# Kernel tuning notes

Measured on AMD Instinct MI355X. Metric: run time of the kernel, lower is better.

The kernel has to match this reference:

```python
import jax, jax.numpy as jnp
from jax import lax
import numpy as np
from jax.scipy.ndimage import map_coordinates

SIGMA = 1.0
RADIUS = 3          # from radius=(3,3); kernel size 7
TAU = (2.0, 2.0)
SCALE_FACTORS = (0.5, 1.0)
ITERATIONS = (2, 2)  # production uses (100,100); reduced for tractable reference
EPS = 1e-9
IN_EPS = 1e-5


def gaussian_kernel1d(sigma, radius):
    x = jnp.arange(-radius, radius + 1, dtype=jnp.float32)
    k = jnp.exp(-0.5 * (x / sigma) ** 2)
    return k / jnp.sum(k)


def smooth3d(vf, k):
    # separable depthwise Gaussian over the 3 spatial axes, SAME padding
    C = vf.shape[1]
    for ax in range(3):
        shp = [1, 1, 1]
        shp[ax] = k.shape[0]
        w = jnp.tile(k.reshape(1, 1, *shp), (C, 1, 1, 1, 1))
        vf = lax.conv_general_dilated(vf, w, (1, 1, 1), 'SAME',
                                      dimension_numbers=('NCDHW', 'OIDHW', 'NCDHW'),
                                      feature_group_count=C)
    return vf


def warp(img, vf):
    # img: [1,1,D,H,W], vf: [1,3,D,H,W] displacement in voxel units
    D, H, W = img.shape[2:]
    gz, gy, gx = jnp.meshgrid(jnp.arange(D, dtype=img.dtype),
                              jnp.arange(H, dtype=img.dtype),
                              jnp.arange(W, dtype=img.dtype), indexing='ij')
    coords = [gz + vf[0, 0], gy + vf[0, 1], gx + vf[0, 2]]
    out = map_coordinates(img[0, 0], coords, order=1, mode='nearest')
    return out[None, None]


def demon_forces(warped, fixed, spacing):
    # active demons: gradient of the (warped) moving image
    diff = warped - fixed  # [1,1,D,H,W]
    g = jnp.stack(jnp.gradient(warped[0, 0]), axis=0)[None]  # [1,3,D,H,W]
    g = g / spacing[None, :, None, None, None]
    denom = jnp.sum(g * g, axis=1, keepdims=True) + diff * diff
    return jnp.where(denom > EPS, diff * g / denom, 0.0)


def match_vf(vf, shape):
    # resize displacement field and rescale its magnitude per axis
    old = vf.shape[2:]
    if tuple(old) == tuple(shape):
        return vf
    scale = jnp.array([s1 / s2 for s1, s2 in zip(shape, old)], jnp.float32)
    vf = jax.image.resize(vf, vf.shape[:2] + tuple(shape), method='trilinear')
    return vf * scale[None, :, None, None, None]


def conv3d(x, w):
    return lax.conv_general_dilated(x, w, (1, 1, 1), 'SAME',
                                    dimension_numbers=('NCDHW', 'OIDHW', 'NCDHW'))


def instance_norm(x):
    m = jnp.mean(x, axis=(2, 3, 4), keepdims=True)
    v = jnp.var(x, axis=(2, 3, 4), keepdims=True)
    return (x - m) / jnp.sqrt(v + IN_EPS)


def mish(x):
    return x * jnp.tanh(jax.nn.softplus(x))


def setup_inputs() -> dict:
    key = jax.random.key(0)
    ks = jax.random.split(key, 8)
    D = 96
    image = jax.random.normal(ks[0], (1, 1, D, D, D), jnp.float32)
    moving = jax.random.normal(ks[1], (1, 1, D, D, D), jnp.float32)
    mask = jnp.ones((1, 1, D, D, D), jnp.float32)
    spacing = jnp.ones((3,), jnp.float32)
    w1 = jax.random.normal(ks[2], (32, 5, 3, 3, 3), jnp.float32) * 0.05
    w2 = jax.random.normal(ks[3], (64, 32, 3, 3, 3), jnp.float32) * 0.05
    w3 = jax.random.normal(ks[4], (32, 64, 3, 3, 3), jnp.float32) * 0.05
    w4 = jax.random.normal(ks[5], (3, 32, 3, 3, 3), jnp.float32) * 0.05
    b4 = jnp.zeros((3,), jnp.float32)
    return {'image': image, 'mask': mask, 'moving': moving, 'spacing': spacing,
            'w1': w1, 'w2': w2, 'w3': w3, 'w4': w4, 'b4': b4}


def reference(image, mask, moving, spacing, w1, w2, w3, w4, b4):
    kernel = gaussian_kernel1d(SIGMA, RADIUS)
    full_shape = image.shape[2:]
    vf = None
    for lvl, (sf, n_it) in enumerate(zip(SCALE_FACTORS, ITERATIONS)):
        shp = tuple(int(s * sf) for s in full_shape)
        f = jax.image.resize(image, image.shape[:2] + shp, method='trilinear')
        m = jax.image.resize(mask, mask.shape[:2] + shp, method='nearest')
        mv = jax.image.resize(moving, moving.shape[:2] + shp, method='trilinear')
        if vf is None:
            vf = jnp.zeros((image.shape[0], 3) + shp, jnp.float32)
        else:
            vf = match_vf(vf, shp)
        tau = TAU[lvl]

        def body(i, vf, mv=mv, f=f, m=m, tau=tau):
            warped = warp(mv, vf)
            vf = vf + tau * demon_forces(warped, f, spacing) * m
            return smooth3d(vf, kernel)

        vf = lax.fori_loop(0, n_it, body, vf)

    # the iterative registration runs under torch.no_grad()
    vf = lax.stop_gradient(vf)
    warped_moving = lax.stop_gradient(warp(moving, vf))  # last level is full scale

    # correction CNN: Conv3d/InstanceNorm3d/Mish stack on [vf, image*mask, warped_moving]
    x = jnp.concatenate([vf, image * mask, warped_moving], axis=1)  # [1,5,D,H,W]
    x = mish(instance_norm(conv3d(x, w1)))
    x = mish(instance_norm(conv3d(x, w2)))
    x = mish(instance_norm(conv3d(x, w3)))
    correction = conv3d(x, w4) + b4[None, :, None, None, None]
    corrected_vf = smooth3d(vf + correction, kernel)

    vf = match_vf(vf, full_shape)
    corrected_vf = match_vf(corrected_vf, full_shape)
    corrected_warped_moving = warp(moving, corrected_vf)
    return corrected_warped_moving, corrected_vf, vf
```

## Files before the change

### kernel.cpp

```cpp
#include <hip/hip_runtime.h>
#include <hip/hip_bf16.h>
#include <math.h>

#define DEV __device__ __forceinline__

constexpr int D96 = 96;
constexpr int N96 = D96 * D96 * D96;
constexpr int D48 = 48;
constexpr int N48 = D48 * D48 * D48;

#define GW0 0.3990502796524549f
#define GW1 0.2420362293761143f
#define GW2 0.05400558262251696f
#define GW3 0.004433048175243745f

typedef __attribute__((ext_vector_type(8))) short s16x8;
typedef __attribute__((ext_vector_type(4))) short s16x4;
typedef __attribute__((ext_vector_type(4))) float f32x4;
typedef __attribute__((ext_vector_type(16))) float f32x16;

DEV int clampi(int v, int lo, int hi) { return v < lo ? lo : (v > hi ? hi : v); }

DEV short f2bf(float f) { __hip_bfloat16 h = __float2bfloat16(f); short s; __builtin_memcpy(&s, &h, 2); return s; }
DEV float bf2f(short s) { __hip_bfloat16 h; __builtin_memcpy(&h, &s, 2); return __bfloat162float(h); }

__global__ void k_downsample2x(const float* __restrict__ src, float* __restrict__ dst)
{
    int idx = blockIdx.x * blockDim.x + threadIdx.x;
    if (idx >= N48) return;
    int x = idx % D48, y = (idx / D48) % D48, z = idx / (D48 * D48);

    float wz[4], wy[4], wx[4];
    int jz[4], jy[4], jx[4];
    auto mk = [](int i, float* w, int* j) {
        const float base[4] = {0.125f, 0.375f, 0.375f, 0.125f};
        float s = 0.f;
        #pragma unroll
        for (int t = 0; t < 4; ++t) {
            int jj = 2 * i - 1 + t;
            bool v = (jj >= 0) && (jj < D96);
            j[t] = v ? jj : 0;
            w[t] = v ? base[t] : 0.f;
            s += w[t];
        }
        float inv = 1.f / s;
        #pragma unroll
        for (int t = 0; t < 4; ++t) w[t] *= inv;
    };
    mk(z, wz, jz); mk(y, wy, jy); mk(x, wx, jx);

    float acc = 0.f;
    #pragma unroll
    for (int a = 0; a < 4; ++a) {
        #pragma unroll
        for (int b = 0; b < 4; ++b) {
            float wab = wz[a] * wy[b];
            int rowoff = (jz[a] * D96 + jy[b]) * D96;
            #pragma unroll
            for (int c = 0; c < 4; ++c)
                acc += wab * wx[c] * src[rowoff + jx[c]];
        }
    }
    dst[idx] = acc;
}

__global__ void k_upsample_vf(const float* __restrict__ src, float* __restrict__ dst)
{
    int idx = blockIdx.x * blockDim.x + threadIdx.x;
    if (idx >= 3 * N96) return;
    int c = idx / N96;
    int s = idx - c * N96;
    int x = s % D96, y = (s / D96) % D96, z = s / (D96 * D96);

    auto mk = [](int i, int* j, float* w) {
        int k = i >> 1;
        if ((i & 1) == 0) { j[0] = k - 1; w[0] = 0.25f; j[1] = k; w[1] = 0.75f; }
        else              { j[0] = k;     w[0] = 0.75f; j[1] = k + 1; w[1] = 0.25f; }
        float sum = 0.f;
        #pragma unroll
        for (int t = 0; t < 2; ++t) {
            bool v = (j[t] >= 0) && (j[t] < D48);
            if (!v) { w[t] = 0.f; j[t] = 0; }
            sum += w[t];
        }
        float inv = 1.f / sum;
        w[0] *= inv; w[1] *= inv;
    };
    int jz[2], jy[2], jx[2]; float wz[2], wy[2], wx[2];
    mk(z, jz, wz); mk(y, jy, wy); mk(x, jx, wx);

    const float* p = src + (size_t)c * N48;
    float acc = 0.f;
    #pragma unroll
    for (int a = 0; a < 2; ++a)
        #pragma unroll
        for (int b = 0; b < 2; ++b) {
            float wab = wz[a] * wy[b];
            int rowoff = (jz[a] * D48 + jy[b]) * D48;
            acc += wab * (wx[0] * p[rowoff + jx[0]] + wx[1] * p[rowoff + jx[1]]);
        }
    dst[idx] = 2.f * acc;
}

__global__ void k_warp(const float* __restrict__ img, const float* __restrict__ vf,
                       float* __restrict__ out, int D)
{
    int N = D * D * D;
    int idx = blockIdx.x * blockDim.x + threadIdx.x;
    if (idx >= N) return;
    int x = idx % D, y = (idx / D) % D, z = idx / (D * D);
    float cz = z + vf[idx], cy = y + vf[N + idx], cx = x + vf[2 * N + idx];
    float fz = floorf(cz), fy = floorf(cy), fx = floorf(cx);
    float wz = cz - fz, wy = cy - fy, wx = cx - fx;
    int z0 = clampi((int)fz, 0, D - 1), z1 = clampi((int)fz + 1, 0, D - 1);
    int y0 = clampi((int)fy, 0, D - 1), y1 = clampi((int)fy + 1, 0, D - 1);
    int x0 = clampi((int)fx, 0, D - 1), x1 = clampi((int)fx + 1, 0, D - 1);
    float v000 = img[(z0 * D + y0) * D + x0], v001 = img[(z0 * D + y0) * D + x1];
    float v010 = img[(z0 * D + y1) * D + x0], v011 = img[(z0 * D + y1) * D + x1];
    float v100 = img[(z1 * D + y0) * D + x0], v101 = img[(z1 * D + y0) * D + x1];
    float v110 = img[(z1 * D + y1) * D + x0], v111 = img[(z1 * D + y1) * D + x1];
    float c00 = v000 + wx * (v001 - v000);
    float c01 = v010 + wx * (v011 - v010);
    float c10 = v100 + wx * (v101 - v100);
    float c11 = v110 + wx * (v111 - v110);
    float c0 = c00 + wy * (c01 - c00);
    float c1 = c10 + wy * (c11 - c10);
    out[idx] = c0 + wz * (c1 - c0);
}

__global__ void k_forces(const float* __restrict__ warped, const float* __restrict__ fixed,
                         const float* __restrict__ mask, const float* __restrict__ spacing,
                         float* __restrict__ vf, int D, int maskD, float tau)
{
    int N = D * D * D;
    int idx = blockIdx.x * blockDim.x + threadIdx.x;
    if (idx >= N) return;
    int x = idx % D, y = (idx / D) % D, z = idx / (D * D);
    float w0 = warped[idx];
    float diff = w0 - fixed[idx];
    int sZ = D * D, sY = D;
    float gz = (z == 0) ? warped[idx + sZ] - w0 : (z == D - 1) ? w0 - warped[idx - sZ]
               : 0.5f * (warped[idx + sZ] - warped[idx - sZ]);
    float gy = (y == 0) ? warped[idx + sY] - w0 : (y == D - 1) ? w0 - warped[idx - sY]
               : 0.5f * (warped[idx + sY] - warped[idx - sY]);
    float gx = (x == 0) ? warped[idx + 1] - w0 : (x == D - 1) ? w0 - warped[idx - 1]
               : 0.5f * (warped[idx + 1] - warped[idx - 1]);
    gz /= spacing[0]; gy /= spacing[1]; gx /= spacing[2];
    float denom = gz * gz + gy * gy + gx * gx + diff * diff;
    float m;
    if (D == maskD) m = mask[idx];
    else {
        float r = (float)maskD / (float)D;
        int mz = clampi((int)((z + 0.5f) * r), 0, maskD - 1);
        int my = clampi((int)((y + 0.5f) * r), 0, maskD - 1);
        int mx = clampi((int)((x + 0.5f) * r), 0, maskD - 1);
        m = mask[(mz * maskD + my) * maskD + mx];
    }
    if (denom > 1e-9f) {
        float sc = tau * diff / denom * m;
        vf[idx]         += sc * gz;
        vf[N + idx]     += sc * gy;
        vf[2 * N + idx] += sc * gx;
    }
}

__global__ __launch_bounds__(256, 2)
void k_smooth3(const float* __restrict__ src, float* __restrict__ dst, int D)
{
    __shared__ float B1[10648];
    __shared__ float B2[7744];
    float* B3 = B1;
    int nt = D >> 4;
    int b = blockIdx.x;
    int tx = b % nt, ty = (b / nt) % nt, tz = b / (nt * nt);
    int c = blockIdx.y;
    int N = D * D * D;
    const float* s = src + (size_t)c * N;
    float* d = dst + (size_t)c * N;
    int x0 = tx * 16, y0 = ty * 16, z0 = tz * 16;
    int tid = threadIdx.x;

    for (int l = tid; l < 10648; l += 256) {
        int xx = l % 22, yy = (l / 22) % 22, zz = l / 484;
        int gz = z0 + zz - 3, gy = y0 + yy - 3, gx = x0 + xx - 3;
        float v = 0.f;
        if ((unsigned)gz < (unsigned)D && (unsigned)gy < (unsigned)D && (unsigned)gx < (unsigned)D)
            v = s[((size_t)gz * D + gy) * D + gx];
        B1[l] = v;
    }
    __syncthreads();
    for (int l = tid; l < 16 * 484; l += 256) {
        int xx = l % 22, yy = (l / 22) % 22, zo = l / 484;
        int base = (zo + 3) * 484 + yy * 22 + xx;
        B2[l] = GW0 * B1[base]
              + GW1 * (B1[base - 484] + B1[base + 484])
              + GW2 * (B1[base - 968] + B1[base + 968])
              + GW3 * (B1[base - 1452] + B1[base + 1452]);
    }
    __syncthreads();
    for (int l = tid; l < 16 * 16 * 22; l += 256) {
        int xx = l % 22, yo = (l / 22) % 16, zo = l / 352;
        int base = zo * 484 + (yo + 3) * 22 + xx;
        B3[l] = GW0 * B2[base]
              + GW1 * (B2[base - 22] + B2[base + 22])
              + GW2 * (B2[base - 44] + B2[base + 44])
              + GW3 * (B2[base - 66] + B2[base + 66]);
    }
    __syncthreads();
    for (int l = tid; l < 4096; l += 256) {
        int xo = l % 16, yo = (l / 16) % 16, zo = l / 256;
        int base = zo * 352 + yo * 22 + xo + 3;
        float a = GW0 * B3[base]
                + GW1 * (B3[base - 1] + B3[base + 1])
                + GW2 * (B3[base - 2] + B3[base + 2])
                + GW3 * (B3[base - 3] + B3[base + 3]);
        d[((size_t)(z0 + zo) * D + (y0 + yo)) * D + (x0 + xo)] = a;
    }
}

__global__ void k_pack_cl(const float* __restrict__ vf, const float* __restrict__ image,
                          const float* __restrict__ mask, const float* __restrict__ warped,
                          short* __restrict__ xin8)
{
    int i = blockIdx.x * blockDim.x + threadIdx.x;
    if (i >= N96) return;
    s16x8 v;
    v[0] = f2bf(vf[i]); v[1] = f2bf(vf[N96 + i]); v[2] = f2bf(vf[2 * N96 + i]);
    v[3] = f2bf(image[i] * mask[i]); v[4] = f2bf(warped[i]);
    v[5] = 0; v[6] = 0; v[7] = 0;
    *reinterpret_cast<s16x8*>(&xin8[(size_t)i * 8]) = v;
}

__global__ void k_wreorder_all(const float* __restrict__ w1, const float* __restrict__ w2,
                               const float* __restrict__ w3, const float* __restrict__ w4,
                               short* __restrict__ r1, short* __restrict__ r2,
                               short* __restrict__ r3, short* __restrict__ r4)
{
    int i = blockIdx.x * 256 + threadIdx.x;
    const int S1 = 7168, S2 = 55296, S3 = 55296, S4 = 13824;
    const float* w; short* r; int CIN, CINP, COUT, COUTP;
    int idx = i;
    if (idx < S1)              { w = w1; r = r1; CIN = 5;  CINP = 8;  COUT = 32; COUTP = 32; }
    else if ((idx -= S1) < S2) { w = w2; r = r2; CIN = 32; CINP = 32; COUT = 64; COUTP = 64; }
    else if ((idx -= S2) < S3) { w = w3; r = r3; CIN = 64; CINP = 64; COUT = 32; COUTP = 32; }
    else if ((idx -= S3) < S4) { w = w4; r = r4; CIN = 32; CINP = 32; COUT = 3;  COUTP = 16; }
    else return;
    int j = idx & 7;
    int co = (idx >> 3) % COUTP;
    int kg = idx / (8 * COUTP);
    int k = kg * 8 + j;
    int off = k / CINP, ci = k % CINP;
    float v = 0.f;
    if (co < COUT && off < 27 && ci < CIN)
        v = w[((size_t)co * CIN + ci) * 27 + off];
    r[idx] = f2bf(v);
}

DEV float mishf(float f)
{
    float e = __expf(f);
    float t = 1.f + e;
    float u = t * t + 1.f;
    return f - 2.f * f * __builtin_amdgcn_rcpf(u);
}

__global__ __launch_bounds__(256, 4)
void k_conv1(const short* __restrict__ act, const short* __restrict__ Wr,
             short* __restrict__ outcl, float* __restrict__ part)
{
    constexpr int YH = 6, TN = 3, KS = 14;
    constexpr int TILE_G = 3 * YH * 98;
    __shared__ __align__(16) short tile[TILE_G * 8];
    float* red = (float*)tile;

    int b = blockIdx.x;
    int xcd = b & 7, bidx = b >> 3;
    int zblk = xcd * 12 + bidx / 24;
    int y0 = (bidx % 24) * 4;

    int tid = threadIdx.x;
    int lane = tid & 63, wave = tid >> 6;
    int ln31 = lane & 31, hi = lane >> 5;

    for (int i = tid; i < TILE_G; i += 256) {
        int xi = i % 98, yi = (i / 98) % YH, zi = i / (98 * YH);
        int gz = zblk + zi - 1, gy = y0 + yi - 1, gx = xi - 1;
        s16x8 v = {0, 0, 0, 0, 0, 0, 0, 0};
        if ((unsigned)gz < 96u && (unsigned)gy < 96u && (unsigned)gx < 96u)
            v = *reinterpret_cast<const s16x8*>(&act[(size_t)((gz * 96 + gy) * 96 + gx) * 8]);
        *reinterpret_cast<s16x8*>(&tile[i * 8]) = v;
    }
    __syncthreads();

    f32x16 acc[TN];
    #pragma unroll
    for (int i = 0; i < TN; ++i)
        #pragma unroll
        for (int e = 0; e < 16; ++e) acc[i][e] = 0.f;

    int xb_[TN];
    #pragma unroll
    for (int i = 0; i < TN; ++i) xb_[i] = i * 32 + ln31;

    #pragma unroll
    for (int ks = 0; ks < KS; ++ks) {
        s16x8 a = *reinterpret_cast<const s16x8*>(&Wr[((size_t)(ks * 2 + hi) * 32 + ln31) * 8]);
        int off = ks * 2 + hi; if (off > 26) off = 26;
        int dz = off / 9, r9 = off - dz * 9, dy = r9 / 3, dx = r9 - dy * 3;
        #pragma unroll
        for (int i = 0; i < TN; ++i) {
            int gi = (dz * YH + wave + dy) * 98 + xb_[i] + dx;
            s16x8 bf = *reinterpret_cast<const s16x8*>(&tile[gi * 8]);
            acc[i] = __builtin_amdgcn_mfma_f32_32x32x16_bf16(a, bf, acc[i], 0, 0, 0);
        }
    }

    float st_s[16], st_q[16];
    #pragma unroll
    for (int j = 0; j < 16; ++j) { st_s[j] = 0.f; st_q[j] = 0.f; }
    #pragma unroll
    for (int i = 0; i < TN; ++i)
        #pragma unroll
        for (int e = 0; e < 16; ++e) {
            float v = acc[i][e];
            st_s[e] += v; st_q[e] += v * v;
        }
    #pragma unroll
    for (int j = 0; j < 16; ++j) {
        #pragma unroll
        for (int o = 1; o <= 16; o <<= 1) {
            st_s[j] += __shfl_xor(st_s[j], o);
            st_q[j] += __shfl_xor(st_q[j], o);
        }
    }

    __syncthreads();
    #pragma unroll
    for (int i = 0; i < TN; ++i) {
        int x = xb_[i];
        #pragma unroll
        for (int q = 0; q < 4; ++q) {
            s16x4 pk;
            #pragma unroll
            for (int r = 0; r < 4; ++r) pk[r] = f2bf(acc[i][q * 4 + r]);
            int bo = (((wave * 96 + x) * 32 + q * 8 + hi * 4) * 2) ^ ((x & 3) << 4);
            *reinterpret_cast<s16x4*>((char*)tile + bo) = pk;
        }
    }
    __syncthreads();
    for (int t = tid; t < 4 * 96 * 4; t += 256) {
        int gran = t & 3;
        int x = (t >> 2) % 96;
        int row = t / (4 * 96);
        int bo = (((row * 96 + x) * 32) * 2 + gran * 16) ^ ((x & 3) << 4);
        s16x8 v = *reinterpret_cast<const s16x8*>((char*)tile + bo);
        int vox = ((zblk * 96) + y0 + row) * 96 + x;
        *reinterpret_cast<s16x8*>(&outcl[(size_t)vox * 32 + gran * 8]) = v;
    }

    __syncthreads();
    if (ln31 == 0) {
        int base = (wave * 2 + hi) * 16;
        #pragma unroll
        for (int j = 0; j < 16; ++j) {
            red[(base + j) * 2]     = st_s[j];
            red[(base + j) * 2 + 1] = st_q[j];
        }
    }
    __syncthreads();
    if (tid < 64) {
        int c = tid >> 1, sel = tid & 1;
        int q = (c >> 3) & 3, hic = (c >> 2) & 1, r = c & 3;
        int j = q * 4 + r;
        float v = 0.f;
        #pragma unroll
        for (int w = 0; w < 4; ++w)
            v += red[((w * 2 + hic) * 16 + j) * 2 + sel];
        part[((size_t)c * gridDim.x + blockIdx.x) * 2 + sel] = v;
    }
}

template <int CINP, int COUTP, int MINW>
__global__ __launch_bounds__(256, MINW)
void k_conv_v3(const short* __restrict__ act, const short* __restrict__ Wr,
               short* __restrict__ outcl, float* __restrict__ part)
{
    constexpr int G = CINP / 8;
    constexpr int HALVES = CINP / 32;
    constexpr int TM = COUTP / 32;
    constexpr int TN = 3;
    constexpr int YH = 6;
    constexpr int TILE_SH = YH * 98 * 32;
    constexpr int TR_SH = 4 * 96 * COUTP;
    constexpr int SH_SIZE = TILE_SH > TR_SH ? TILE_SH : TR_SH;
    __shared__ __align__(16) short tile[SH_SIZE];
    float* red = (float*)tile;

    int b = blockIdx.x;
    int xcd = b & 7, bidx = b >> 3;
    int zblk = xcd * 12 + bidx / 24;
    int y0 = (bidx % 24) * 4;

    int tid = threadIdx.x;
    int lane = tid & 63, wave = tid >> 6;
    int ln31 = lane & 31, hi = lane >> 5;

    int xb_[TN];
    #pragma unroll
    for (int i = 0; i < TN; ++i) xb_[i] = i * 32 + ln31;

    f32x16 acc[TN][TM];
    #pragma unroll
    for (int i = 0; i < TN; ++i)
        #pragma unroll
        for (int m = 0; m < TM; ++m)
            #pragma unroll
            for (int e = 0; e < 16; ++e) acc[i][m][e] = 0.f;

    for (int p = 0; p < 3; ++p) {
        int gz = zblk + p - 1;
        for (int h = 0; h < HALVES; ++h) {
            __syncthreads();
            for (int i = tid; i < YH * 98 * 4; i += 256) {
                int g = i & 3, xi = (i >> 2) % 98, yi = (i >> 2) / 98;
                int gy = y0 + yi - 1, gx = xi - 1;
                s16x8 v = {0, 0, 0, 0, 0, 0, 0, 0};
                if ((unsigned)gz < 96u && (unsigned)gy < 96u && (unsigned)gx < 96u)
                    v = *reinterpret_cast<const s16x8*>(
                        &act[(size_t)((gz * 96 + gy) * 96 + gx) * CINP + (h * 4 + g) * 8]);
                int slot = g ^ ((xi >> 1) & 3);
                *reinterpret_cast<s16x8*>(&tile[(((yi * 98 + xi) << 2) + slot) * 8]) = v;
            }
            __syncthreads();
            int kgbase = p * 9 * G + h * 4;
            #pragma unroll
            for (int ks = 0; ks < 18; ++ks) {
                int kg = kgbase + (ks >> 1) * G + (ks & 1) * 2 + hi;
                s16x8 A[TM];
                #pragma unroll
                for (int m = 0; m < TM; ++m)
                    A[m] = *reinterpret_cast<const s16x8*>(
                        &Wr[((size_t)kg * COUTP + m * 32 + ln31) * 8]);
                int dy = (ks >> 1) / 3, dx = (ks >> 1) % 3;
                int gl = (ks & 1) * 2 + hi;
                #pragma unroll
                for (int i = 0; i < TN; ++i) {
                    int xi = xb_[i] + dx;
                    int gi = (((wave + dy) * 98 + xi) << 2) + (gl ^ ((xi >> 1) & 3));
                    s16x8 bf = *reinterpret_cast<const s16x8*>(&tile[gi * 8]);
                    #pragma unroll
                    for (int m = 0; m < TM; ++m)
                        acc[i][m] = __builtin_amdgcn_mfma_f32_32x32x16_bf16(A[m], bf, acc[i][m], 0, 0, 0);
                }
            }
        }
    }

    float st_s[TM * 16], st_q[TM * 16];
    #pragma unroll
    for (int j = 0; j < TM * 16; ++j) { st_s[j] = 0.f; st_q[j] = 0.f; }
    #pragma unroll
    for (int i = 0; i < TN; ++i)
        #pragma unroll
        for (int m = 0; m < TM; ++m)
            #pragma unroll
            for (int e = 0; e < 16; ++e) {
                float v = acc[i][m][e];
                st_s[m * 16 + e] += v;
                st_q[m * 16 + e] += v * v;
            }
    #pragma unroll
    for (int j = 0; j < TM * 16; ++j) {
        #pragma unroll
        for (int o = 1; o <= 16; o <<= 1) {
            st_s[j] += __shfl_xor(st_s[j], o);
            st_q[j] += __shfl_xor(st_q[j], o);
        }
    }

    constexpr int XM = (COUTP == 64) ? 7 : 3;
    __syncthreads();
    #pragma unroll
    for (int i = 0; i < TN; ++i) {
        int x = xb_[i];
        #pragma unroll
        for (int m = 0; m < TM; ++m)
            #pragma unroll
            for (int q = 0; q < 4; ++q) {
                s16x4 pk;
                #pragma unroll
                for (int r = 0; r < 4; ++r) pk[r] = f2bf(acc[i][m][q * 4 + r]);
                int bo = (((wave * 96 + x) * COUTP + m * 32 + q * 8 + hi * 4) * 2) ^ ((x & XM) << 4);
                *reinterpret_cast<s16x4*>((char*)tile + bo) = pk;
            }
    }
    __syncthreads();
    constexpr int GR = COUTP / 8;
    for (int t = tid; t < 4 * 96 * GR; t += 256) {
        int gran = t % GR;
        int x = (t / GR) % 96;
        int row = t / (GR * 96);
        int bo = (((row * 96 + x) * COUTP) * 2 + gran * 16) ^ ((x & XM) << 4);
        s16x8 v = *reinterpret_cast<const s16x8*>((char*)tile + bo);
        int vox = ((zblk * 96) + y0 + row) * 96 + x;
        *reinterpret_cast<s16x8*>(&outcl[(size_t)vox * COUTP + gran * 8]) = v;
    }

    __syncthreads();
    if (ln31 == 0) {
        int base = (wave * 2 + hi) * (TM * 16);
        #pragma unroll
        for (int j = 0; j < TM * 16; ++j) {
            red[(base + j) * 2]     = st_s[j];
            red[(base + j) * 2 + 1] = st_q[j];
        }
    }
    __syncthreads();
    if (tid < COUTP * 2) {
        int c = tid >> 1, sel = tid & 1;
        int m = c >> 5, q = (c >> 3) & 3, hic = (c >> 2) & 1, r = c & 3;
        int j = m * 16 + q * 4 + r;
        float v = 0.f;
        #pragma unroll
        for (int w = 0; w < 4; ++w)
            v += red[((w * 2 + hic) * (TM * 16) + j) * 2 + sel];
        part[((size_t)c * gridDim.x + blockIdx.x) * 2 + sel] = v;
    }
}

__global__ __launch_bounds__(256, 4)
void k_conv4(const short* __restrict__ act, const short* __restrict__ Wr,
             const float* __restrict__ bias, const float* __restrict__ vf,
             float* __restrict__ corr, float* __restrict__ outvf)
{
    constexpr int YH = 6;
    __shared__ __align__(16) short tile[YH * 98 * 32];

    int b = blockIdx.x;
    int xcd = b & 7, bidx = b >> 3;
    int zblk = xcd * 12 + bidx / 24;
    int y0 = (bidx % 24) * 4;

    int tid = threadIdx.x;
    int lane = tid & 63, wave = tid >> 6;
    int ln15 = lane & 15, lg = lane >> 4;

    f32x4 acc[6];
    #pragma unroll
    for (int i = 0; i < 6; ++i) acc[i] = {0.f, 0.f, 0.f, 0.f};

    for (int p = 0; p < 3; ++p) {
        int gz = zblk + p - 1;
        __syncthreads();
        for (int i = tid; i < YH * 98 * 4; i += 256) {
            int g = i & 3, xi = (i >> 2) % 98, yi = (i >> 2) / 98;
            int gy = y0 + yi - 1, gx = xi - 1;
            s16x8 v = {0, 0, 0, 0, 0, 0, 0, 0};
            if ((unsigned)gz < 96u && (unsigned)gy < 96u && (unsigned)gx < 96u)
                v = *reinterpret_cast<const s16x8*>(
                    &act[(size_t)((gz * 96 + gy) * 96 + gx) * 32 + g * 8]);
            int slot = g ^ ((xi >> 1) & 3);
            *reinterpret_cast<s16x8*>(&tile[(((yi * 98 + xi) << 2) + slot) * 8]) = v;
        }
        __syncthreads();
        #pragma unroll
        for (int ks = 0; ks < 9; ++ks) {
            int kg = (p * 9 + ks) * 4 + lg;
            s16x8 a = *reinterpret_cast<const s16x8*>(&Wr[((size_t)kg * 16 + ln15) * 8]);
            int dy = ks / 3, dx = ks % 3;
            #pragma unroll
            for (int i = 0; i < 6; ++i) {
                int xi = i * 16 + ln15 + dx;
                int gi = (((wave + dy) * 98 + xi) << 2) + (lg ^ ((xi >> 1) & 3));
                s16x8 bf = *reinterpret_cast<const s16x8*>(&tile[gi * 8]);
                acc[i] = __builtin_amdgcn_mfma_f32_16x16x32_bf16(a, bf, acc[i], 0, 0, 0);
            }
        }
    }
    if (lg == 0) {
        #pragma unroll
        for (int i = 0; i < 6; ++i) {
            int vox = ((zblk * 96) + y0 + wave) * 96 + i * 16 + ln15;
            #pragma unroll
            for (int r = 0; r < 3; ++r) {
                float v = vf[(size_t)r * N96 + vox];
                corr[(size_t)r * N96 + vox] = acc[i][r] + bias[r] + v;
                outvf[(size_t)r * N96 + vox] = v;
            }
        }
    }
}

template <int C>
__global__ void k_norm_mish_cl(short* __restrict__ x, const float* __restrict__ stats)
{
    constexpr int G8 = C / 8;
    int gt = blockIdx.x * 256 + threadIdx.x;
    int cg = threadIdx.x % G8;
    float mean[8], inv[8];
    #pragma unroll
    for (int j = 0; j < 8; ++j) { mean[j] = stats[2 * (cg * 8 + j)]; inv[j] = stats[2 * (cg * 8 + j) + 1]; }
    const int TGn = N96 * G8;
    int stride = gridDim.x * 256;
    for (int i = gt; i < TGn; i += stride) {
        s16x8 v = *reinterpret_cast<const s16x8*>(&x[(size_t)i * 8]);
        #pragma unroll
        for (int j = 0; j < 8; ++j)
            v[j] = f2bf(mishf((bf2f(v[j]) - mean[j]) * inv[j]));
        *reinterpret_cast<s16x8*>(&x[(size_t)i * 8]) = v;
    }
}

__global__ void k_stats_reduce(const float* __restrict__ part, float* __restrict__ stats,
                               int G, int N)
{
    int c = blockIdx.x;
    int t = threadIdx.x;
    float s = 0.f, s2 = 0.f;
    for (int i = t; i < G; i += blockDim.x) {
        s  += part[((size_t)c * G + i) * 2];
        s2 += part[((size_t)c * G + i) * 2 + 1];
    }
    #pragma unroll
    for (int o = 32; o > 0; o >>= 1) { s += __shfl_down(s, o); s2 += __shfl_down(s2, o); }
    __shared__ float a[4], b[4];
    int lane = t & 63, wid = t >> 6;
    if (lane == 0) { a[wid] = s; b[wid] = s2; }
    __syncthreads();
    if (t == 0) {
        float ss = a[0] + a[1] + a[2] + a[3];
        float qq = b[0] + b[1] + b[2] + b[3];
        float mean = ss / (float)N;
        float var = qq / (float)N - mean * mean;
        stats[2 * c] = mean;
        stats[2 * c + 1] = rsqrtf(var + 1e-5f);
    }
}

extern "C" void kernel_launch(void* const* d_in, const int* in_sizes, int n_in,
                              void* d_out, int out_size, void* d_ws, size_t ws_size,
                              hipStream_t stream)
{
    const float* image   = (const float*)d_in[0];
    const float* mask    = (const float*)d_in[1];
    const float* moving  = (const float*)d_in[2];
    const float* spacing = (const float*)d_in[3];
    const float* w1 = (const float*)d_in[4];
    const float* w2 = (const float*)d_in[5];
    const float* w3 = (const float*)d_in[6];
    const float* w4 = (const float*)d_in[7];
    const float* b4 = (const float*)d_in[8];
    float* out = (float*)d_out;

    char* ws = (char*)d_ws;
    size_t off = 0;
    auto alloc = [&](size_t bytes) -> char* {
        char* p = ws + off;
        off += (bytes + 255) & ~(size_t)255;
        return p;
    };
    float* f48   = (float*)alloc((size_t)N48 * 4);
    float* mv48  = (float*)alloc((size_t)N48 * 4);
    float* vfA48 = (float*)alloc((size_t)3 * N48 * 4);
    float* vfB48 = (float*)alloc((size_t)3 * N48 * 4);
    float* wrp48 = (float*)alloc((size_t)N48 * 4);
    float* vfA96 = (float*)alloc((size_t)3 * N96 * 4);
    float* vfB96 = (float*)alloc((size_t)3 * N96 * 4);
    float* vfC96 = (float*)alloc((size_t)3 * N96 * 4);
    float* wrp96 = (float*)alloc((size_t)N96 * 4);
    short* xin8  = (short*)alloc((size_t)8 * N96 * 2);
    short* y1    = (short*)alloc((size_t)32 * N96 * 2);
    short* y2    = (short*)alloc((size_t)64 * N96 * 2);
    short* wr1   = (short*)alloc((size_t)7168 * 2);
    short* wr2   = (short*)alloc((size_t)55296 * 2);
    short* wr3   = (short*)alloc((size_t)55296 * 2);
    short* wr4   = (short*)alloc((size_t)13824 * 2);
    float* part  = (float*)alloc((size_t)64 * 2304 * 2 * 4);
    float* stats = (float*)alloc((size_t)64 * 2 * 4);

    const int B = 256;
    const int g48  = (N48 + B - 1) / B;
    const int g96  = (N96 + B - 1) / B;
    const int g96c = (3 * N96 + B - 1) / B;

    k_wreorder_all<<<(131584 + 255) / 256, B, 0, stream>>>(w1, w2, w3, w4, wr1, wr2, wr3, wr4);

    k_downsample2x<<<g48, B, 0, stream>>>(image, f48);
    k_downsample2x<<<g48, B, 0, stream>>>(moving, mv48);
    hipMemsetAsync(vfA48, 0, (size_t)3 * N48 * 4, stream);
    float* cur = vfA48; float* oth = vfB48;
    for (int it = 0; it < 2; ++it) {
        k_warp<<<g48, B, 0, stream>>>(mv48, cur, wrp48, D48);
        k_forces<<<g48, B, 0, stream>>>(wrp48, f48, mask, spacing, cur, D48, D96, 2.0f);
        k_smooth3<<<dim3(27, 3), B, 0, stream>>>(cur, oth, D48);
        float* tmp = cur; cur = oth; oth = tmp;
    }

    k_upsample_vf<<<g96c, B, 0, stream>>>(cur, vfA96);
    float* cur9 = vfA96; float* oth9 = vfB96;
    for (int it = 0; it < 2; ++it) {
        k_warp<<<g96, B, 0, stream>>>(moving, cur9, wrp96, D96);
        k_forces<<<g96, B, 0, stream>>>(wrp96, image, mask, spacing, cur9, D96, D96, 2.0f);
        k_smooth3<<<dim3(216, 3), B, 0, stream>>>(cur9, oth9, D96);
        float* tmp = cur9; cur9 = oth9; oth9 = tmp;
    }

    k_warp<<<g96, B, 0, stream>>>(moving, cur9, wrp96, D96);
    k_pack_cl<<<g96, B, 0, stream>>>(cur9, image, mask, wrp96, xin8);

    k_conv1<<<2304, B, 0, stream>>>(xin8, wr1, y1, part);
    k_stats_reduce<<<32, B, 0, stream>>>(part, stats, 2304, N96);
    k_norm_mish_cl<32><<<2048, B, 0, stream>>>(y1, stats);

    k_conv_v3<32, 64, 3><<<2304, B, 0, stream>>>(y1, wr2, y2, part);
    k_stats_reduce<<<64, B, 0, stream>>>(part, stats, 2304, N96);
    k_norm_mish_cl<64><<<2048, B, 0, stream>>>(y2, stats);

    k_conv_v3<64, 32, 4><<<2304, B, 0, stream>>>(y2, wr3, y1, part);
    k_stats_reduce<<<32, B, 0, stream>>>(part, stats, 2304, N96);
    k_norm_mish_cl<32><<<2048, B, 0, stream>>>(y1, stats);

    k_conv4<<<2304, B, 0, stream>>>(y1, wr4, b4, cur9, vfC96, out + (size_t)4 * N96);

    k_smooth3<<<dim3(216, 3), B, 0, stream>>>(vfC96, out + N96, D96);

    k_warp<<<g96, B, 0, stream>>>(moving, out + N96, out, D96);
}
```

Before: 806.8 us.

## Use direct global-to-LDS loads and double-buffer conv input tiles

Replaces the register-staged global→LDS tile loads in the conv kernels with global_load_lds 16-byte direct copies. Out-of-bounds voxels read from a small zeroed buffer. The middle conv layers are restructured into finer 16-channel phases with a double-buffered LDS tile and software prefetch of weights, so the next tile loads while MFMAs run on the current one. Occupancy hints drop to 3 waves per SIMD, and the swizzle changes to fit the 2-slot layout. The main risks are that lower occupancy and smaller phases with more barriers could offset the overlap gains.

Measured after the change: 886.9 us. 9.9% more time.

```diff
diff --git a/kernel.cpp b/kernel.cpp
--- a/kernel.cpp
+++ b/kernel.cpp
@@ -18,6 +18,10 @@
 typedef __attribute__((ext_vector_type(4))) short s16x4;
 typedef __attribute__((ext_vector_type(4))) float f32x4;
 typedef __attribute__((ext_vector_type(16))) float f32x16;
+
+#define GLD16(src, dst) __builtin_amdgcn_global_load_lds( \
+    (const __attribute__((address_space(1))) void*)(src), \
+    (__attribute__((address_space(3))) void*)(dst), 16, 0, 0)
 
 DEV int clampi(int v, int lo, int hi) { return v < lo ? lo : (v > hi ? hi : v); }
 
@@ -266,11 +270,11 @@
 
 __global__ __launch_bounds__(256, 4)
 void k_conv1(const short* __restrict__ act, const short* __restrict__ Wr,
-             short* __restrict__ outcl, float* __restrict__ part)
+             short* __restrict__ outcl, float* __restrict__ part,
+             const short* __restrict__ zbuf)
 {
     constexpr int YH = 6, TN = 3, KS = 14;
-    constexpr int TILE_G = 3 * YH * 98;
-    __shared__ __align__(16) short tile[TILE_G * 8];
+    __shared__ __align__(16) short tile[1792 * 8];
     float* red = (float*)tile;
 
     int b = blockIdx.x;
@@ -282,13 +286,17 @@
     int lane = tid & 63, wave = tid >> 6;
     int ln31 = lane & 31, hi = lane >> 5;
 
-    for (int i = tid; i < TILE_G; i += 256) {
-        int xi = i % 98, yi = (i / 98) % YH, zi = i / (98 * YH);
-        int gz = zblk + zi - 1, gy = y0 + yi - 1, gx = xi - 1;
-        s16x8 v = {0, 0, 0, 0, 0, 0, 0, 0};
-        if ((unsigned)gz < 96u && (unsigned)gy < 96u && (unsigned)gx < 96u)
-            v = *reinterpret_cast<const s16x8*>(&act[(size_t)((gz * 96 + gy) * 96 + gx) * 8]);
-        *reinterpret_cast<s16x8*>(&tile[i * 8]) = v;
+    #pragma unroll
+    for (int it = 0; it < 7; ++it) {
+        int i = it * 256 + tid;
+        const short* src = zbuf;
+        if (i < 1764) {
+            int xi = i % 98, yi = (i / 98) % YH, zi = i / (98 * YH);
+            int gz = zblk + zi - 1, gy = y0 + yi - 1, gx = xi - 1;
+            if ((unsigned)gz < 96u && (unsigned)gy < 96u && (unsigned)gx < 96u)
+                src = &act[(size_t)((gz * 96 + gy) * 96 + gx) * 8];
+        }
+        GLD16(src, &tile[(it * 256 + wave * 64) * 8]);
     }
     __syncthreads();
 
@@ -380,20 +388,21 @@
     }
 }
 
-template <int CINP, int COUTP, int MINW>
-__global__ __launch_bounds__(256, MINW)
-void k_conv_v3(const short* __restrict__ act, const short* __restrict__ Wr,
-               short* __restrict__ outcl, float* __restrict__ part)
+template <int CINP, int COUTP>
+__global__ __launch_bounds__(256, 3)
+void k_conv_v4(const short* __restrict__ act, const short* __restrict__ Wr,
+               short* __restrict__ outcl, float* __restrict__ part,
+               const short* __restrict__ zbuf)
 {
     constexpr int G = CINP / 8;
-    constexpr int HALVES = CINP / 32;
+    constexpr int HALVES = CINP / 16;
+    constexpr int P = 3 * HALVES;
     constexpr int TM = COUTP / 32;
     constexpr int TN = 3;
-    constexpr int YH = 6;
-    constexpr int TILE_SH = YH * 98 * 32;
+    constexpr int BUFG = 1280;
     constexpr int TR_SH = 4 * 96 * COUTP;
-    constexpr int SH_SIZE = TILE_SH > TR_SH ? TILE_SH : TR_SH;
-    __shared__ __align__(16) short tile[SH_SIZE];
+    constexpr int SH = (2 * BUFG * 8 > TR_SH) ? 2 * BUFG * 8 : TR_SH;
+    __shared__ __align__(16) short tile[SH];
     float* red = (float*)tile;
 
     int b = blockIdx.x;
@@ -417,43 +426,62 @@
             #pragma unroll
             for (int e = 0; e < 16; ++e) acc[i][m][e] = 0.f;
 
-    for (int p = 0; p < 3; ++p) {
+    auto stage = [&](int ph, int bb) {
+        int p = ph / HALVES, h = ph - (ph / HALVES) * HALVES;
         int gz = zblk + p - 1;
-        for (int h = 0; h < HALVES; ++h) {
-            __syncthreads();
-            for (int i = tid; i < YH * 98 * 4; i += 256) {
-                int g = i & 3, xi = (i >> 2) % 98, yi = (i >> 2) / 98;
+        short* dst0 = &tile[bb * (BUFG * 8)];
+        #pragma unroll
+        for (int it = 0; it < 5; ++it) {
+            int i = it * 256 + tid;
+            const short* src = zbuf;
+            if (i < 1176) {
+                int sl = i & 1, x2 = i >> 1;
+                int xi = x2 % 98, yi = x2 / 98;
                 int gy = y0 + yi - 1, gx = xi - 1;
-                s16x8 v = {0, 0, 0, 0, 0, 0, 0, 0};
-                if ((unsigned)gz < 96u && (unsigned)gy < 96u && (unsigned)gx < 96u)
-                    v = *reinterpret_cast<const s16x8*>(
-                        &act[(size_t)((gz * 96 + gy) * 96 + gx) * CINP + (h * 4 + g) * 8]);
-                int slot = g ^ ((xi >> 1) & 3);
-                *reinterpret_cast<s16x8*>(&tile[(((yi * 98 + xi) << 2) + slot) * 8]) = v;
+                if ((unsigned)gz < 96u && (unsigned)gy < 96u && (unsigned)gx < 96u) {
+                    int g = sl ^ (((xi >> 1) ^ (xi >> 2) ^ (xi >> 3)) & 1);
+                    src = &act[(size_t)((gz * 96 + gy) * 96 + gx) * CINP + (h * 2 + g) * 8];
+                }
             }
-            __syncthreads();
-            int kgbase = p * 9 * G + h * 4;
-            #pragma unroll
-            for (int ks = 0; ks < 18; ++ks) {
-                int kg = kgbase + (ks >> 1) * G + (ks & 1) * 2 + hi;
-                s16x8 A[TM];
+            GLD16(src, &dst0[(it * 256 + wave * 64) * 8]);
+        }
+    };
+
+    stage(0, 0);
+    __syncthreads();
+
+    for (int ph = 0; ph < P; ++ph) {
+        int bb = ph & 1;
+        if (ph + 1 < P) stage(ph + 1, bb ^ 1);
+        int p = ph / HALVES, h = ph - (ph / HALVES) * HALVES;
+        const short* tb = &tile[bb * (BUFG * 8)];
+        int kg0 = p * 9 * G + h * 2 + hi;
+        s16x8 Ac[TM], An[TM];
+        #pragma unroll
+        for (int m = 0; m < TM; ++m)
+            Ac[m] = *reinterpret_cast<const s16x8*>(&Wr[((size_t)kg0 * COUTP + m * 32 + ln31) * 8]);
+        #pragma unroll
+        for (int ks = 0; ks < 9; ++ks) {
+            if (ks + 1 < 9) {
+                int kg = kg0 + (ks + 1) * G;
                 #pragma unroll
                 for (int m = 0; m < TM; ++m)
-                    A[m] = *reinterpret_cast<const s16x8*>(
-                        &Wr[((size_t)kg * COUTP + m * 32 + ln31) * 8]);
-                int dy = (ks >> 1) / 3, dx = (ks >> 1) % 3;
-                int gl = (ks & 1) * 2 + hi;
+                    An[m] = *reinterpret_cast<const s16x8*>(&Wr[((size_t)kg * COUTP + m * 32 + ln31) * 8]);
+            }
+            int dy = ks / 3, dx = ks % 3;
+            #pragma unroll
+            for (int i = 0; i < TN; ++i) {
+                int xi = xb_[i] + dx;
+                int gi = ((wave + dy) * 98 + xi) * 2 + (hi ^ (((xi >> 1) ^ (xi >> 2) ^ (xi >> 3)) & 1));
+                s16x8 bf = *reinterpret_cast<const s16x8*>(&tb[gi * 8]);
                 #pragma unroll
-                for (int i = 0; i < TN; ++i) {
-                    int xi = xb_[i] + dx;
-                    int gi = (((wave + dy) * 98 + xi) << 2) + (gl ^ ((xi >> 1) & 3));
-                    s16x8 bf = *reinterpret_cast<const s16x8*>(&tile[gi * 8]);
-                    #pragma unroll
-                    for (int m = 0; m < TM; ++m)
-                        acc[i][m] = __builtin_amdgcn_mfma_f32_32x32x16_bf16(A[m], bf, acc[i][m], 0, 0, 0);
-                }
+                for (int m = 0; m < TM; ++m)
+                    acc[i][m] = __builtin_amdgcn_mfma_f32_32x32x16_bf16(Ac[m], bf, acc[i][m], 0, 0, 0);
             }
-        }
+            #pragma unroll
+            for (int m = 0; m < TM; ++m) Ac[m] = An[m];
+        }
+        __syncthreads();
     }
 
     float st_s[TM * 16], st_q[TM * 16];
@@ -479,7 +507,6 @@
     }
 
     constexpr int XM = (COUTP == 64) ? 7 : 3;
-    __syncthreads();
     #pragma unroll
     for (int i = 0; i < TN; ++i) {
         int x = xb_[i];
@@ -528,13 +555,14 @@
     }
 }
 
-__global__ __launch_bounds__(256, 4)
+__global__ __launch_bounds__(256, 3)
 void k_conv4(const short* __restrict__ act, const short* __restrict__ Wr,
              const float* __restrict__ bias, const float* __restrict__ vf,
-             float* __restrict__ corr, float* __restrict__ outvf)
+             float* __restrict__ corr, float* __restrict__ outvf,
+             const short* __restrict__ zbuf)
 {
     constexpr int YH = 6;
-    __shared__ __align__(16) short tile[YH * 98 * 32];
+    __shared__ __align__(16) short tile[2560 * 8];
 
     int b = blockIdx.x;
     int xcd = b & 7, bidx = b >> 3;
@@ -552,15 +580,20 @@
     for (int p = 0; p < 3; ++p) {
         int gz = zblk + p - 1;
         __syncthreads();
-        for (int i = tid; i < YH * 98 * 4; i += 256) {
-            int g = i & 3, xi = (i >> 2) % 98, yi = (i >> 2) / 98;
-            int gy = y0 + yi - 1, gx = xi - 1;
-            s16x8 v = {0, 0, 0, 0, 0, 0, 0, 0};
-            if ((unsigned)gz < 96u && (unsigned)gy < 96u && (unsigned)gx < 96u)
-                v = *reinterpret_cast<const s16x8*>(
-                    &act[(size_t)((gz * 96 + gy) * 96 + gx) * 32 + g * 8]);
-            int slot = g ^ ((xi >> 1) & 3);
-            *reinterpret_cast<s16x8*>(&tile[(((yi * 98 + xi) << 2) + slot) * 8]) = v;
+        #pragma unroll
+        for (int it = 0; it < 10; ++it) {
+            int i = it * 256 + tid;
+            const short* src = zbuf;
+            if (i < 2352) {
+                int sl = i & 3, x2 = i >> 2;
+                int xi = x2 % 98, yi = x2 / 98;
+                int gy = y0 + yi - 1, gx = xi - 1;
+                if ((unsigned)gz < 96u && (unsigned)gy < 96u && (unsigned)gx < 96u) {
+                    int g = sl ^ ((xi >> 1) & 3);
+                    src = &act[(size_t)((gz * 96 + gy) * 96 + gx) * 32 + g * 8];
+                }
+            }
+            GLD16(src, &tile[(it * 256 + wave * 64) * 8]);
         }
         __syncthreads();
         #pragma unroll
@@ -677,11 +710,14 @@
     short* wr4   = (short*)alloc((size_t)13824 * 2);
     float* part  = (float*)alloc((size_t)64 * 2304 * 2 * 4);
     float* stats = (float*)alloc((size_t)64 * 2 * 4);
+    short* zbuf  = (short*)alloc(256);
 
     const int B = 256;
     const int g48  = (N48 + B - 1) / B;
     const int g96  = (N96 + B - 1) / B;
     const int g96c = (3 * N96 + B - 1) / B;
+
+    hipMemsetAsync(zbuf, 0, 256, stream);
 
     k_wreorder_all<<<(131584 + 255) / 256, B, 0, stream>>>(w1, w2, w3, w4, wr1, wr2, wr3, wr4);
 
@@ -708,19 +744,19 @@
     k_warp<<<g96, B, 0, stream>>>(moving, cur9, wrp96, D96);
     k_pack_cl<<<g96, B, 0, stream>>>(cur9, image, mask, wrp96, xin8);
 
-    k_conv1<<<2304, B, 0, stream>>>(xin8, wr1, y1, part);
+    k_conv1<<<2304, B, 0, stream>>>(xin8, wr1, y1, part, zbuf);
     k_stats_reduce<<<32, B, 0, stream>>>(part, stats, 2304, N96);
     k_norm_mish_cl<32><<<2048, B, 0, stream>>>(y1, stats);
 
-    k_conv_v3<32, 64, 3><<<2304, B, 0, stream>>>(y1, wr2, y2, part);
+    k_conv_v4<32, 64><<<2304, B, 0, stream>>>(y1, wr2, y2, part, zbuf);
     k_stats_reduce<<<64, B, 0, stream>>>(part, stats, 2304, N96);
     k_norm_mish_cl<64><<<2048, B, 0, stream>>>(y2, stats);
 
-    k_conv_v3<64, 32, 4><<<2304, B, 0, stream>>>(y2, wr3, y1, part);
+    k_conv_v4<64, 32><<<2304, B, 0, stream>>>(y2, wr3, y1, part, zbuf);
     k_stats_reduce<<<32, B, 0, stream>>>(part, stats, 2304, N96);
     k_norm_mish_cl<32><<<2048, B, 0, stream>>>(y1, stats);
 
-    k_conv4<<<2304, B, 0, stream>>>(y1, wr4, b4, cur9, vfC96, out + (size_t)4 * N96);
+    k_conv4<<<2304, B, 0, stream>>>(y1, wr4, b4, cur9, vfC96, out + (size_t)4 * N96, zbuf);
 
     k_smooth3<<<dim3(216, 3), B, 0, stream>>>(vfC96, out + N96, D96);
 
```

## Split conv2/conv3 output channels across two blocks, use 16x16 MFMA for conv3

Applied to the files above, without the earlier changes.

Replaces the templated conv kernel with two specialised kernels that each compute half the output channels per block, doubling the grid to 4608 blocks. Conv2 keeps 32x32 MFMA tiles but holds a single accumulator set. Conv3 moves to 16x16x32 MFMA with 16 output channels per block. The aim is to cut register pressure and raise occupancy and parallelism, at the cost of each block reloading the input tile, which doubles activation reads from global memory.

Result: faster. 784.6 us (-2.8%).

```diff
diff --git a/kernel.cpp b/kernel.cpp
--- a/kernel.cpp
+++ b/kernel.cpp
@@ -380,23 +380,17 @@
     }
 }
 
-template <int CINP, int COUTP, int MINW>
-__global__ __launch_bounds__(256, MINW)
-void k_conv_v3(const short* __restrict__ act, const short* __restrict__ Wr,
+__global__ __launch_bounds__(256, 4)
+void k_conv_c2(const short* __restrict__ act, const short* __restrict__ Wr,
                short* __restrict__ outcl, float* __restrict__ part)
 {
-    constexpr int G = CINP / 8;
-    constexpr int HALVES = CINP / 32;
-    constexpr int TM = COUTP / 32;
-    constexpr int TN = 3;
-    constexpr int YH = 6;
-    constexpr int TILE_SH = YH * 98 * 32;
-    constexpr int TR_SH = 4 * 96 * COUTP;
-    constexpr int SH_SIZE = TILE_SH > TR_SH ? TILE_SH : TR_SH;
-    __shared__ __align__(16) short tile[SH_SIZE];
+    constexpr int TN = 3, YH = 6;
+    __shared__ __align__(16) short tile[YH * 98 * 32];
     float* red = (float*)tile;
 
-    int b = blockIdx.x;
+    int bb = blockIdx.x;
+    int ch = bb & 1;
+    int b = bb >> 1;
     int xcd = b & 7, bidx = b >> 3;
     int zblk = xcd * 12 + bidx / 24;
     int y0 = (bidx % 24) * 4;
@@ -409,17 +403,135 @@
     #pragma unroll
     for (int i = 0; i < TN; ++i) xb_[i] = i * 32 + ln31;
 
-    f32x16 acc[TN][TM];
+    f32x16 acc[TN];
     #pragma unroll
     for (int i = 0; i < TN; ++i)
         #pragma unroll
-        for (int m = 0; m < TM; ++m)
-            #pragma unroll
-            for (int e = 0; e < 16; ++e) acc[i][m][e] = 0.f;
+        for (int e = 0; e < 16; ++e) acc[i][e] = 0.f;
 
     for (int p = 0; p < 3; ++p) {
         int gz = zblk + p - 1;
-        for (int h = 0; h < HALVES; ++h) {
+        __syncthreads();
+        for (int i = tid; i < YH * 98 * 4; i += 256) {
+            int g = i & 3, xi = (i >> 2) % 98, yi = (i >> 2) / 98;
+            int gy = y0 + yi - 1, gx = xi - 1;
+            s16x8 v = {0, 0, 0, 0, 0, 0, 0, 0};
+            if ((unsigned)gz < 96u && (unsigned)gy < 96u && (unsigned)gx < 96u)
+                v = *reinterpret_cast<const s16x8*>(
+                    &act[(size_t)((gz * 96 + gy) * 96 + gx) * 32 + g * 8]);
+            int slot = g ^ ((xi >> 1) & 3);
+            *reinterpret_cast<s16x8*>(&tile[(((yi * 98 + xi) << 2) + slot) * 8]) = v;
+        }
+        __syncthreads();
+        int kgbase = p * 36;
+        #pragma unroll
+        for (int ks = 0; ks < 18; ++ks) {
+            int kg = kgbase + (ks >> 1) * 4 + (ks & 1) * 2 + hi;
+            s16x8 A = *reinterpret_cast<const s16x8*>(
+                &Wr[((size_t)kg * 64 + ch * 32 + ln31) * 8]);
+            int dy = (ks >> 1) / 3, dx = (ks >> 1) % 3;
+            int gl = (ks & 1) * 2 + hi;
+            #pragma unroll
+            for (int i = 0; i < TN; ++i) {
+                int xi = xb_[i] + dx;
+                int gi = (((wave + dy) * 98 + xi) << 2) + (gl ^ ((xi >> 1) & 3));
+                s16x8 bf = *reinterpret_cast<const s16x8*>(&tile[gi * 8]);
+                acc[i] = __builtin_amdgcn_mfma_f32_32x32x16_bf16(A, bf, acc[i], 0, 0, 0);
+            }
+        }
+    }
+
+    float st_s[16], st_q[16];
+    #pragma unroll
+    for (int j = 0; j < 16; ++j) { st_s[j] = 0.f; st_q[j] = 0.f; }
+    #pragma unroll
+    for (int i = 0; i < TN; ++i)
+        #pragma unroll
+        for (int e = 0; e < 16; ++e) {
+            float v = acc[i][e];
+            st_s[e] += v; st_q[e] += v * v;
+        }
+    #pragma unroll
+    for (int j = 0; j < 16; ++j) {
+        #pragma unroll
+        for (int o = 1; o <= 16; o <<= 1) {
+            st_s[j] += __shfl_xor(st_s[j], o);
+            st_q[j] += __shfl_xor(st_q[j], o);
+        }
+    }
+
+    __syncthreads();
+    #pragma unroll
+    for (int i = 0; i < TN; ++i) {
+        int x = xb_[i];
+        #pragma unroll
+        for (int q = 0; q < 4; ++q) {
+            s16x4 pk;
+            #pragma unroll
+            for (int r = 0; r < 4; ++r) pk[r] = f2bf(acc[i][q * 4 + r]);
+            int bo = (((wave * 96 + x) * 32 + q * 8 + hi * 4) * 2) ^ ((x & 3) << 4);
+            *reinterpret_cast<s16x4*>((char*)tile + bo) = pk;
+        }
+    }
+    __syncthreads();
+    for (int t = tid; t < 4 * 96 * 4; t += 256) {
+        int gran = t & 3;
+        int x = (t >> 2) % 96;
+        int row = t / (4 * 96);
+        int bo = (((row * 96 + x) * 32) * 2 + gran * 16) ^ ((x & 3) << 4);
+        s16x8 v = *reinterpret_cast<const s16x8*>((char*)tile + bo);
+        int vox = ((zblk * 96) + y0 + row) * 96 + x;
+        *reinterpret_cast<s16x8*>(&outcl[(size_t)vox * 64 + ch * 32 + gran * 8]) = v;
+    }
+
+    __syncthreads();
+    if (ln31 == 0) {
+        int base = (wave * 2 + hi) * 16;
+        #pragma unroll
+        for (int j = 0; j < 16; ++j) {
+            red[(base + j) * 2]     = st_s[j];
+            red[(base + j) * 2 + 1] = st_q[j];
+        }
+    }
+    __syncthreads();
+    if (tid < 64) {
+        int c = tid >> 1, sel = tid & 1;
+        int q = (c >> 3) & 3, hic = (c >> 2) & 1, r = c & 3;
+        int j = q * 4 + r;
+        float v = 0.f;
+        #pragma unroll
+        for (int w = 0; w < 4; ++w)
+            v += red[((w * 2 + hic) * 16 + j) * 2 + sel];
+        part[((size_t)(ch * 32 + c) * 2304 + b) * 2 + sel] = v;
+    }
+}
+
+__global__ __launch_bounds__(256, 4)
+void k_conv_c3(const short* __restrict__ act, const short* __restrict__ Wr,
+               short* __restrict__ outcl, float* __restrict__ part)
+{
+    constexpr int YH = 6;
+    __shared__ __align__(16) short tile[YH * 98 * 32];
+    float* red = (float*)tile;
+
+    int bb = blockIdx.x;
+    int ch = bb & 1;
+    int b = bb >> 1;
+    int xcd = b & 7, bidx = b >> 3;
+    int zblk = xcd * 12 + bidx / 24;
+    int y0 = (bidx % 24) * 4;
+
+    int tid = threadIdx.x;
+    int lane = tid & 63, wave = tid >> 6;
+    int ln15 = lane & 15, lg = lane >> 4;
+
+    f32x4 acc[6];
+    #pragma unroll
+    for (int i = 0; i < 6; ++i) acc[i] = {0.f, 0.f, 0.f, 0.f};
+
+    for (int p = 0; p < 3; ++p) {
+        int gz = zblk + p - 1;
+        for (int h = 0; h < 2; ++h) {
             __syncthreads();
             for (int i = tid; i < YH * 98 * 4; i += 256) {
                 int g = i & 3, xi = (i >> 2) % 98, yi = (i >> 2) / 98;
@@ -427,104 +539,85 @@
                 s16x8 v = {0, 0, 0, 0, 0, 0, 0, 0};
                 if ((unsigned)gz < 96u && (unsigned)gy < 96u && (unsigned)gx < 96u)
                     v = *reinterpret_cast<const s16x8*>(
-                        &act[(size_t)((gz * 96 + gy) * 96 + gx) * CINP + (h * 4 + g) * 8]);
+                        &act[(size_t)((gz * 96 + gy) * 96 + gx) * 64 + (h * 4 + g) * 8]);
                 int slot = g ^ ((xi >> 1) & 3);
                 *reinterpret_cast<s16x8*>(&tile[(((yi * 98 + xi) << 2) + slot) * 8]) = v;
             }
             __syncthreads();
-            int kgbase = p * 9 * G + h * 4;
             #pragma unroll
-            for (int ks = 0; ks < 18; ++ks) {
-                int kg = kgbase + (ks >> 1) * G + (ks & 1) * 2 + hi;
-                s16x8 A[TM];
+            for (int off = 0; off < 9; ++off) {
+                int kg = (p * 9 + off) * 8 + h * 4 + lg;
+                s16x8 A = *reinterpret_cast<const s16x8*>(
+                    &Wr[((size_t)kg * 32 + ch * 16 + ln15) * 8]);
+                int dy = off / 3, dx = off % 3;
                 #pragma unroll
-                for (int m = 0; m < TM; ++m)
-                    A[m] = *reinterpret_cast<const s16x8*>(
-                        &Wr[((size_t)kg * COUTP + m * 32 + ln31) * 8]);
-                int dy = (ks >> 1) / 3, dx = (ks >> 1) % 3;
-                int gl = (ks & 1) * 2 + hi;
-                #pragma unroll
-                for (int i = 0; i < TN; ++i) {
-                    int xi = xb_[i] + dx;
-                    int gi = (((wave + dy) * 98 + xi) << 2) + (gl ^ ((xi >> 1) & 3));
+                for (int i = 0; i < 6; ++i) {
+                    int xi = i * 16 + ln15 + dx;
+                    int gi = (((wave + dy) * 98 + xi) << 2) + (lg ^ ((xi >> 1) & 3));
                     s16x8 bf = *reinterpret_cast<const s16x8*>(&tile[gi * 8]);
-                    #pragma unroll
-                    for (int m = 0; m < TM; ++m)
-                        acc[i][m] = __builtin_amdgcn_mfma_f32_32x32x16_bf16(A[m], bf, acc[i][m], 0, 0, 0);
+                    acc[i] = __builtin_amdgcn_mfma_f32_16x16x32_bf16(A, bf, acc[i], 0, 0, 0);
                 }
             }
         }
     }
 
-    float st_s[TM * 16], st_q[TM * 16];
-    #pragma unroll
-    for (int j = 0; j < TM * 16; ++j) { st_s[j] = 0.f; st_q[j] = 0.f; }
-    #pragma unroll
-    for (int i = 0; i < TN; ++i)
-        #pragma unroll
-        for (int m = 0; m < TM; ++m)
-            #pragma unroll
-            for (int e = 0; e < 16; ++e) {
-                float v = acc[i][m][e];
-                st_s[m * 16 + e] += v;
-                st_q[m * 16 + e] += v * v;
-            }
-    #pragma unroll
-    for (int j = 0; j < TM * 16; ++j) {
-        #pragma unroll
-        for (int o = 1; o <= 16; o <<= 1) {
+    float st_s[4], st_q[4];
+    #pragma unroll
+    for (int j = 0; j < 4; ++j) { st_s[j] = 0.f; st_q[j] = 0.f; }
+    #pragma unroll
+    for (int i = 0; i < 6; ++i)
+        #pragma unroll
+        for (int r = 0; r < 4; ++r) {
+            float v = acc[i][r];
+            st_s[r] += v; st_q[r] += v * v;
+        }
+    #pragma unroll
+    for (int j = 0; j < 4; ++j) {
+        #pragma unroll
+        for (int o = 1; o <= 8; o <<= 1) {
             st_s[j] += __shfl_xor(st_s[j], o);
             st_q[j] += __shfl_xor(st_q[j], o);
         }
     }
 
-    constexpr int XM = (COUTP == 64) ? 7 : 3;
-    __syncthreads();
-    #pragma unroll
-    for (int i = 0; i < TN; ++i) {
-        int x = xb_[i];
-        #pragma unroll
-        for (int m = 0; m < TM; ++m)
-            #pragma unroll
-            for (int q = 0; q < 4; ++q) {
-                s16x4 pk;
-                #pragma unroll
-                for (int r = 0; r < 4; ++r) pk[r] = f2bf(acc[i][m][q * 4 + r]);
-                int bo = (((wave * 96 + x) * COUTP + m * 32 + q * 8 + hi * 4) * 2) ^ ((x & XM) << 4);
-                *reinterpret_cast<s16x4*>((char*)tile + bo) = pk;
-            }
-    }
-    __syncthreads();
-    constexpr int GR = COUTP / 8;
-    for (int t = tid; t < 4 * 96 * GR; t += 256) {
-        int gran = t % GR;
-        int x = (t / GR) % 96;
-        int row = t / (GR * 96);
-        int bo = (((row * 96 + x) * COUTP) * 2 + gran * 16) ^ ((x & XM) << 4);
+    __syncthreads();
+    #pragma unroll
+    for (int i = 0; i < 6; ++i) {
+        int x = i * 16 + ln15;
+        s16x4 pk;
+        #pragma unroll
+        for (int r = 0; r < 4; ++r) pk[r] = f2bf(acc[i][r]);
+        int bo = (((wave * 96 + x) * 16 + lg * 4) * 2) ^ ((x & 3) << 4);
+        *reinterpret_cast<s16x4*>((char*)tile + bo) = pk;
+    }
+    __syncthreads();
+    for (int t = tid; t < 4 * 96 * 2; t += 256) {
+        int gran = t & 1;
+        int x = (t >> 1) % 96;
+        int row = t / (2 * 96);
+        int bo = (((row * 96 + x) * 16) * 2 + gran * 16) ^ ((x & 3) << 4);
         s16x8 v = *reinterpret_cast<const s16x8*>((char*)tile + bo);
         int vox = ((zblk * 96) + y0 + row) * 96 + x;
-        *reinterpret_cast<s16x8*>(&outcl[(size_t)vox * COUTP + gran * 8]) = v;
-    }
-
-    __syncthreads();
-    if (ln31 == 0) {
-        int base = (wave * 2 + hi) * (TM * 16);
-        #pragma unroll
-        for (int j = 0; j < TM * 16; ++j) {
+        *reinterpret_cast<s16x8*>(&outcl[(size_t)vox * 32 + ch * 16 + gran * 8]) = v;
+    }
+
+    __syncthreads();
+    if (ln15 == 0) {
+        int base = (wave * 4 + lg) * 4;
+        #pragma unroll
+        for (int j = 0; j < 4; ++j) {
             red[(base + j) * 2]     = st_s[j];
             red[(base + j) * 2 + 1] = st_q[j];
         }
     }
     __syncthreads();
-    if (tid < COUTP * 2) {
+    if (tid < 32) {
         int c = tid >> 1, sel = tid & 1;
-        int m = c >> 5, q = (c >> 3) & 3, hic = (c >> 2) & 1, r = c & 3;
-        int j = m * 16 + q * 4 + r;
         float v = 0.f;
         #pragma unroll
         for (int w = 0; w < 4; ++w)
-            v += red[((w * 2 + hic) * (TM * 16) + j) * 2 + sel];
-        part[((size_t)c * gridDim.x + blockIdx.x) * 2 + sel] = v;
+            v += red[((w * 4 + (c >> 2)) * 4 + (c & 3)) * 2 + sel];
+        part[((size_t)(ch * 16 + c) * 2304 + b) * 2 + sel] = v;
     }
 }
 
@@ -712,11 +805,11 @@
     k_stats_reduce<<<32, B, 0, stream>>>(part, stats, 2304, N96);
     k_norm_mish_cl<32><<<2048, B, 0, stream>>>(y1, stats);
 
-    k_conv_v3<32, 64, 3><<<2304, B, 0, stream>>>(y1, wr2, y2, part);
+    k_conv_c2<<<4608, B, 0, stream>>>(y1, wr2, y2, part);
     k_stats_reduce<<<64, B, 0, stream>>>(part, stats, 2304, N96);
     k_norm_mish_cl<64><<<2048, B, 0, stream>>>(y2, stats);
 
-    k_conv_v3<64, 32, 4><<<2304, B, 0, stream>>>(y2, wr3, y1, part);
+    k_conv_c3<<<4608, B, 0, stream>>>(y2, wr3, y1, part);
     k_stats_reduce<<<32, B, 0, stream>>>(part, stats, 2304, N96);
     k_norm_mish_cl<32><<<2048, B, 0, stream>>>(y1, stats);
 
```
